# Optimization experiments

Measured on AMD Instinct MI355X. Metric: run time of the kernel, lower is better.

The kernel has to match this reference:

```python
import jax, jax.numpy as jnp
import numpy as np

D_MODEL, D_Q, D_K, D_V, N = 1024, 128, 128, 128, 8192

def setup_inputs() -> dict:
    key = jax.random.key(0)
    ks = jax.random.split(key, 7)
    s = 1.0 / np.sqrt(D_MODEL)
    return {
        "x": jax.random.normal(ks[0], (N, D_MODEL), dtype=jnp.float32),
        "Wq": jax.random.uniform(ks[1], (D_MODEL, D_Q), jnp.float32, -s, s),
        "bq": jax.random.uniform(ks[2], (D_Q,), jnp.float32, -s, s),
        "Wk": jax.random.uniform(ks[3], (D_MODEL, D_K), jnp.float32, -s, s),
        "bk": jax.random.uniform(ks[4], (D_K,), jnp.float32, -s, s),
        "Wv": jax.random.uniform(ks[5], (D_MODEL, D_V), jnp.float32, -s, s),
        "bv": jax.random.uniform(ks[6], (D_V,), jnp.float32, -s, s),
    }

def reference(x, Wq, bq, Wk, bk, Wv, bv):
    q = x @ Wq + bq          # [N, d_q]
    k = x @ Wk + bk          # [N, d_k]
    v = x @ Wv + bv          # [N, d_v]
    scale = jnp.sqrt(jnp.asarray(q.shape[-1], q.dtype))
    scores = (q @ k.T) / scale          # [N, N]
    attn = jax.nn.softmax(scores, axis=1)  # matches nn.Softmax(dim=1) on 2D
    return attn @ v                     # [N, d_v]
```

## Files before the change

kernel.cpp:

```cpp
#include <hip/hip_runtime.h>


typedef __attribute__((ext_vector_type(8))) short bf16x8;
typedef __attribute__((ext_vector_type(4))) float f32x4;

#define NTOK 8192
#define DMODEL 1024
#define DH 128
#define NSPLIT 8
#define CPS 16

__device__ __forceinline__ unsigned short f2bf(float f) {
  unsigned int u = __builtin_bit_cast(unsigned int, f);
  u += 0x7fffu + ((u >> 16) & 1u);
  return (unsigned short)(u >> 16);
}

__device__ __forceinline__ unsigned int pack2bf(float a, float b) {
  return (unsigned int)f2bf(a) | ((unsigned int)f2bf(b) << 16);
}

__device__ __forceinline__ void gl2lds16(const void* gp, void* lp) {
  const __attribute__((address_space(1))) unsigned int* g =
      (const __attribute__((address_space(1))) unsigned int*)gp;
  __attribute__((address_space(3))) unsigned int* l =
      (__attribute__((address_space(3))) unsigned int*)lp;
  __builtin_amdgcn_global_load_lds(g, l, 16, 0, 0);
}

__global__ __launch_bounds__(256) void k_prep(const float* __restrict__ x,
                                              const float* __restrict__ Wq,
                                              const float* __restrict__ Wk,
                                              const float* __restrict__ Wv,
                                              unsigned short* __restrict__ xb,
                                              unsigned short* __restrict__ wt) {
  __shared__ unsigned short tile[32 * 130];
  int bid = blockIdx.x;
  int t = threadIdx.x;
  if (bid < 4096) {
    int gid = bid * 256 + t;
    const float4* src = (const float4*)x;
    float4 a = src[2 * gid];
    float4 b = src[2 * gid + 1];
    union { unsigned short s[8]; uint4 v; } o;
    o.s[0] = f2bf(a.x); o.s[1] = f2bf(a.y); o.s[2] = f2bf(a.z); o.s[3] = f2bf(a.w);
    o.s[4] = f2bf(b.x); o.s[5] = f2bf(b.y); o.s[6] = f2bf(b.z); o.s[7] = f2bf(b.w);
    ((uint4*)xb)[gid] = o.v;
  } else {
    int b2 = bid - 4096;
    int p = b2 >> 5;
    int k0 = (b2 & 31) * 32;
    const float* W = (p == 0) ? Wq : ((p == 1) ? Wk : Wv);
    float vscale = (p == 2) ? 0.0625f : 1.0f;
#pragma unroll
    for (int i = 0; i < 16; i++) {
      int e = i * 256 + t;
      int n = e & 127, kk = e >> 7;
      tile[kk * 130 + n] = f2bf(W[(size_t)(k0 + kk) * DH + n] * vscale);
    }
    __syncthreads();
#pragma unroll
    for (int i = 0; i < 16; i++) {
      int e = i * 256 + t;
      int kk = e & 31, n = e >> 5;
      wt[(size_t)(p * DH + n) * DMODEL + k0 + kk] = tile[kk * 130 + n];
    }
  }
}

__global__ __launch_bounds__(256) void k_qkv(const unsigned short* __restrict__ xb,
                                             const unsigned short* __restrict__ wt,
                                             const float* __restrict__ bq,
                                             const float* __restrict__ bk,
                                             const float* __restrict__ bv,
                                             unsigned short* __restrict__ qs,
                                             unsigned short* __restrict__ kkv,
                                             unsigned short* __restrict__ vt) {
  __shared__ unsigned short xt[2][64 * 64];
  __shared__ unsigned short wtt[2][128 * 64];
  int p = blockIdx.x, mt = blockIdx.y;
  int tid = threadIdx.x;
  int w = tid >> 6, lane = tid & 63, l16 = lane & 15, g = lane >> 4;

#define STAGE_Q(buf, k0)                                                     \
  {                                                                          \
    _Pragma("unroll") for (int ii = 0; ii < 2; ii++) {                       \
      int i = w * 2 + ii;                                                    \
      int xrow = i * 8 + (lane >> 3);                                        \
      int xpc = (lane & 7) ^ (xrow & 7);                                     \
      gl2lds16(&xb[(size_t)(mt * 64 + xrow) * DMODEL + (k0) + xpc * 8],      \
               &xt[buf][i * 512]);                                           \
    }                                                                        \
    _Pragma("unroll") for (int ii = 0; ii < 4; ii++) {                       \
      int i = w * 4 + ii;                                                    \
      int wr = i * 8 + (lane >> 3);                                          \
      int wpc = (lane & 7) ^ (wr & 7);                                       \
      gl2lds16(&wt[(size_t)(p * DH + wr) * DMODEL + (k0) + wpc * 8],         \
               &wtt[buf][i * 512]);                                          \
    }                                                                        \
  }

  f32x4 zero = {0.f, 0.f, 0.f, 0.f};
  f32x4 acc[8];
#pragma unroll
  for (int i = 0; i < 8; i++) acc[i] = zero;

  STAGE_Q(0, 0);
  int arow = w * 16 + l16, r7 = l16 & 7;

  for (int kt2 = 0; kt2 < 16; kt2++) {
    int b = kt2 & 1;
    __syncthreads();
    if (kt2 < 15) STAGE_Q(b ^ 1, (kt2 + 1) * 64);

    bf16x8 a0 = *(const bf16x8*)&xt[b][arow * 64 + ((g ^ r7) & 7) * 8];
    bf16x8 a1 = *(const bf16x8*)&xt[b][arow * 64 + (((4 + g) ^ r7) & 7) * 8];
#pragma unroll
    for (int nt = 0; nt < 8; nt++) {
      int col = nt * 16 + l16;
      int c7 = col & 7;
      bf16x8 b0 = *(const bf16x8*)&wtt[b][col * 64 + ((g ^ c7) & 7) * 8];
      bf16x8 b1 = *(const bf16x8*)&wtt[b][col * 64 + (((4 + g) ^ c7) & 7) * 8];
      acc[nt] = __builtin_amdgcn_mfma_f32_16x16x32_bf16(a0, b0, acc[nt], 0, 0, 0);
      acc[nt] = __builtin_amdgcn_mfma_f32_16x16x32_bf16(a1, b1, acc[nt], 0, 0, 0);
    }
  }
#undef STAGE_Q

  const float* bias = (p == 0) ? bq : ((p == 1) ? bk : bv);
  float mult = (p == 0) ? (0.08838834764831845f * 1.44269504088896340f) : 1.0f;
  if (p < 2) {
    unsigned short* outp = (p == 0) ? qs : kkv;
#pragma unroll
    for (int nt = 0; nt < 8; nt++) {
      int col = nt * 16 + l16;
      float bsv = bias[col];
#pragma unroll
      for (int r = 0; r < 4; r++) {
        int row = mt * 64 + w * 16 + g * 4 + r;
        outp[(size_t)row * DH + col] = f2bf((acc[nt][r] + bsv) * mult);
      }
    }
  } else {
#pragma unroll
    for (int nt = 0; nt < 8; nt++) {
      int col = nt * 16 + l16;
      float bsv = bias[col] * 0.0625f;
      int row0 = mt * 64 + w * 16 + g * 4;
      uint2 uv;
      uv.x = pack2bf(acc[nt][0] + bsv, acc[nt][1] + bsv);
      uv.y = pack2bf(acc[nt][2] + bsv, acc[nt][3] + bsv);
      *(uint2*)(&vt[(size_t)col * NTOK + row0]) = uv;
    }
  }
}

__global__ __launch_bounds__(256, 2) void k_flash(const unsigned short* __restrict__ qs,
                                                  const unsigned short* __restrict__ kkv,
                                                  const unsigned short* __restrict__ vt,
                                                  _Float16* __restrict__ opart,
                                                  float* __restrict__ lpart) {
  __shared__ unsigned short kt[2][64 * 128];
  __shared__ unsigned short vtl[2][128 * 64];
  __shared__ unsigned short pscr[4 * 2 * 1024];
  int sp = blockIdx.x, qt = blockIdx.y;
  int tid = threadIdx.x;
  int w = tid >> 6, lane = tid & 63, l16 = lane & 15, g = lane >> 4;
  int swz2 = (l16 & 7) ^ ((l16 >> 3) << 1);

  bf16x8 qf[2][4];
  int qbase = qt * 128 + w * 32;
#pragma unroll
  for (int q2 = 0; q2 < 2; q2++)
#pragma unroll
    for (int f = 0; f < 4; f++)
      qf[q2][f] = *(const bf16x8*)(&qs[(size_t)(qbase + q2 * 16 + l16) * DH + f * 32 + g * 8]);

  int pcK[4], pcV[2], pcP[2];
#pragma unroll
  for (int f = 0; f < 4; f++) {
    int lc = f * 4 + g;
    pcK[f] = (lc & 8) | ((lc ^ l16) & 7);
  }
#pragma unroll
  for (int kb = 0; kb < 2; kb++) {
    int lc = kb * 4 + g;
    pcV[kb] = (lc ^ l16) & 7;
    pcP[kb] = (lc ^ swz2) & 7;
  }

#define STAGE_FLASH(buf, chunk)                                                 \
  {                                                                             \
    int key0 = (chunk) * 64;                                                    \
    _Pragma("unroll") for (int ii = 0; ii < 4; ii++) {                          \
      int i = w * 4 + ii;                                                       \
      int krow = 4 * i + (lane >> 4);                                           \
      int klc = ((lane & 15) & 8) | (((lane & 15) ^ krow) & 7);                 \
      gl2lds16(&kkv[(size_t)(key0 + krow) * DH + klc * 8], &kt[buf][i * 512]);  \
      int vrow = 8 * i + (lane >> 3);                                           \
      int vlc = ((lane & 7) ^ vrow) & 7;                                        \
      gl2lds16(&vt[(size_t)vrow * NTOK + key0 + vlc * 8], &vtl[buf][i * 512]);  \
    }                                                                           \
  }

  f32x4 zero = {0.f, 0.f, 0.f, 0.f};
  f32x4 o[2][8];
#pragma unroll
  for (int q2 = 0; q2 < 2; q2++)
#pragma unroll
    for (int dt = 0; dt < 8; dt++) o[q2][dt] = zero;
  float l[2] = {0.f, 0.f};

  int c0 = sp * CPS;
  STAGE_FLASH(0, c0);

  for (int it = 0; it < CPS; it++) {
    int b = it & 1;
    __syncthreads();
    if (it + 1 < CPS) STAGE_FLASH(b ^ 1, c0 + it + 1);

    f32x4 s[2][4];
#pragma unroll
    for (int q2 = 0; q2 < 2; q2++)
#pragma unroll
      for (int mt = 0; mt < 4; mt++) s[q2][mt] = zero;
#pragma unroll
    for (int mt = 0; mt < 4; mt++) {
      bf16x8 kf[4];
#pragma unroll
      for (int f = 0; f < 4; f++)
        kf[f] = *(const bf16x8*)(&kt[b][(mt * 16 + l16) * 128 + pcK[f] * 8]);
#pragma unroll
      for (int f = 0; f < 4; f++) {
        s[0][mt] = __builtin_amdgcn_mfma_f32_16x16x32_bf16(kf[f], qf[0][f], s[0][mt], 0, 0, 0);
        s[1][mt] = __builtin_amdgcn_mfma_f32_16x16x32_bf16(kf[f], qf[1][f], s[1][mt], 0, 0, 0);
      }
    }

#pragma unroll
    for (int q2 = 0; q2 < 2; q2++) {
      unsigned short* pw = &pscr[(w * 2 + q2) * 1024];
      float ssum = 0.f;
#pragma unroll
      for (int mt = 0; mt < 4; mt++) {
        float p0 = __builtin_amdgcn_exp2f(s[q2][mt][0]);
        float p1 = __builtin_amdgcn_exp2f(s[q2][mt][1]);
        float p2 = __builtin_amdgcn_exp2f(s[q2][mt][2]);
        float p3 = __builtin_amdgcn_exp2f(s[q2][mt][3]);
        ssum += (p0 + p1) + (p2 + p3);
        uint2 uv;
        uv.x = pack2bf(p0, p1);
        uv.y = pack2bf(p2, p3);
        int ch = ((mt * 2 + (g >> 1)) ^ swz2) & 7;
        *(uint2*)(&pw[l16 * 64 + ch * 8 + (g & 1) * 4]) = uv;
      }
      l[q2] += ssum;
    }

    bf16x8 pb[2][2];
#pragma unroll
    for (int q2 = 0; q2 < 2; q2++)
#pragma unroll
      for (int kb = 0; kb < 2; kb++)
        pb[q2][kb] = *(const bf16x8*)(&pscr[(w * 2 + q2) * 1024 + l16 * 64 + pcP[kb] * 8]);

#pragma unroll
    for (int dt = 0; dt < 8; dt++)
#pragma unroll
      for (int kb = 0; kb < 2; kb++) {
        bf16x8 vf = *(const bf16x8*)(&vtl[b][(dt * 16 + l16) * 64 + pcV[kb] * 8]);
        o[0][dt] = __builtin_amdgcn_mfma_f32_16x16x32_bf16(vf, pb[0][kb], o[0][dt], 0, 0, 0);
        o[1][dt] = __builtin_amdgcn_mfma_f32_16x16x32_bf16(vf, pb[1][kb], o[1][dt], 0, 0, 0);
      }
  }
#undef STAGE_FLASH

#pragma unroll
  for (int q2 = 0; q2 < 2; q2++) {
    l[q2] += __shfl_xor(l[q2], 16);
    l[q2] += __shfl_xor(l[q2], 32);
    int qrow = qbase + q2 * 16 + l16;
    size_t obase = ((size_t)sp * NTOK + qrow) * DH;
#pragma unroll
    for (int dt = 0; dt < 8; dt++) {
      union { _Float16 h[4]; uint2 u; } pk;
      pk.h[0] = (_Float16)o[q2][dt][0];
      pk.h[1] = (_Float16)o[q2][dt][1];
      pk.h[2] = (_Float16)o[q2][dt][2];
      pk.h[3] = (_Float16)o[q2][dt][3];
      *(uint2*)(&opart[obase + dt * 16 + g * 4]) = pk.u;
    }
    if (g == 0) lpart[sp * NTOK + qrow] = l[q2];
  }
}

__global__ __launch_bounds__(256) void k_merge(const _Float16* __restrict__ opart,
                                               const float* __restrict__ lpart,
                                               float* __restrict__ out) {
  int gid = blockIdx.x * 256 + threadIdx.x;
  int row = gid >> 6, cp = gid & 63;
  float den = 0.f, n0 = 0.f, n1 = 0.f;
#pragma unroll
  for (int s = 0; s < NSPLIT; s++) {
    den += lpart[s * NTOK + row];
    union { unsigned int u; _Float16 h[2]; } v;
    v.u = *(const unsigned int*)&opart[((size_t)s * NTOK + row) * DH + cp * 2];
    n0 += (float)v.h[0];
    n1 += (float)v.h[1];
  }
  float inv = 16.0f / den;
  *(float2*)&out[(size_t)row * DH + cp * 2] = make_float2(n0 * inv, n1 * inv);
}

extern "C" void kernel_launch(void* const* d_in, const int* in_sizes, int n_in,
                              void* d_out, int out_size, void* d_ws, size_t ws_size,
                              hipStream_t stream) {
  const float* x  = (const float*)d_in[0];
  const float* Wq = (const float*)d_in[1];
  const float* bq = (const float*)d_in[2];
  const float* Wk = (const float*)d_in[3];
  const float* bk = (const float*)d_in[4];
  const float* Wv = (const float*)d_in[5];
  const float* bv = (const float*)d_in[6];
  float* out = (float*)d_out;

  char* ws = (char*)d_ws;
  unsigned short* xb    = (unsigned short*)(ws);
  _Float16*       opart = (_Float16*)(ws);
  unsigned short* wt  = (unsigned short*)(ws + 16777216);
  unsigned short* qsb = (unsigned short*)(ws + 17563648);
  unsigned short* kkb = (unsigned short*)(ws + 19660800);
  unsigned short* vtb = (unsigned short*)(ws + 21757952);
  float* lpart = (float*)(ws + 23855104);

  k_prep<<<4192, 256, 0, stream>>>(x, Wq, Wk, Wv, xb, wt);
  k_qkv<<<dim3(3, 128), 256, 0, stream>>>(xb, wt, bq, bk, bv, qsb, kkb, vtb);
  k_flash<<<dim3(NSPLIT, 64), 256, 0, stream>>>(qsb, kkb, vtb, opart, lpart);
  k_merge<<<2048, 256, 0, stream>>>(opart, lpart, out);
}
```

Baseline: 158.2 us.

## Shrink flash key chunks to 32 and raise split count and occupancy

Halves the per-iteration key/value tile in the flash kernel from 64 to 32 keys and reworks the LDS swizzles and the padded P scratch to match. This cuts shared memory per block, so launch bounds rise from 2 to 3 blocks per CU. The key range is now split 12 ways instead of 8, with uneven chunk boundaries, to fill the extra slots. Workspace offsets move to fit the larger partial-output buffer. In exchange there are more barriers per key processed, more partial outputs for the merge kernel to combine, and tighter register limits.

```diff
diff --git a/kernel.cpp b/kernel.cpp
--- a/kernel.cpp
+++ b/kernel.cpp
@@ -7,8 +7,8 @@
 #define NTOK 8192
 #define DMODEL 1024
 #define DH 128
-#define NSPLIT 8
-#define CPS 16
+#define NSPLIT 12
+#define NCH32 256
 
 __device__ __forceinline__ unsigned short f2bf(float f) {
   unsigned int u = __builtin_bit_cast(unsigned int, f);
@@ -155,18 +155,18 @@
   }
 }
 
-__global__ __launch_bounds__(256, 2) void k_flash(const unsigned short* __restrict__ qs,
+__global__ __launch_bounds__(256, 3) void k_flash(const unsigned short* __restrict__ qs,
                                                   const unsigned short* __restrict__ kkv,
                                                   const unsigned short* __restrict__ vt,
                                                   _Float16* __restrict__ opart,
                                                   float* __restrict__ lpart) {
-  __shared__ unsigned short kt[2][64 * 128];
-  __shared__ unsigned short vtl[2][128 * 64];
-  __shared__ unsigned short pscr[4 * 2 * 1024];
+  __shared__ unsigned short kt[2][32 * 128];
+  __shared__ unsigned short vtl[2][128 * 32];
+  __shared__ unsigned short pscr[4 * 2 * 640];
   int sp = blockIdx.x, qt = blockIdx.y;
   int tid = threadIdx.x;
   int w = tid >> 6, lane = tid & 63, l16 = lane & 15, g = lane >> 4;
-  int swz2 = (l16 & 7) ^ ((l16 >> 3) << 1);
+  int l3 = l16 & 3;
 
   bf16x8 qf[2][4];
   int qbase = qt * 128 + w * 32;
@@ -176,31 +176,27 @@
     for (int f = 0; f < 4; f++)
       qf[q2][f] = *(const bf16x8*)(&qs[(size_t)(qbase + q2 * 16 + l16) * DH + f * 32 + g * 8]);
 
-  int pcK[4], pcV[2], pcP[2];
+  int pcK[4];
 #pragma unroll
   for (int f = 0; f < 4; f++) {
     int lc = f * 4 + g;
     pcK[f] = (lc & 8) | ((lc ^ l16) & 7);
   }
-#pragma unroll
-  for (int kb = 0; kb < 2; kb++) {
-    int lc = kb * 4 + g;
-    pcV[kb] = (lc ^ l16) & 7;
-    pcP[kb] = (lc ^ swz2) & 7;
-  }
-
-#define STAGE_FLASH(buf, chunk)                                                 \
-  {                                                                             \
-    int key0 = (chunk) * 64;                                                    \
-    _Pragma("unroll") for (int ii = 0; ii < 4; ii++) {                          \
-      int i = w * 4 + ii;                                                       \
-      int krow = 4 * i + (lane >> 4);                                           \
-      int klc = ((lane & 15) & 8) | (((lane & 15) ^ krow) & 7);                 \
-      gl2lds16(&kkv[(size_t)(key0 + krow) * DH + klc * 8], &kt[buf][i * 512]);  \
-      int vrow = 8 * i + (lane >> 3);                                           \
-      int vlc = ((lane & 7) ^ vrow) & 7;                                        \
-      gl2lds16(&vt[(size_t)vrow * NTOK + key0 + vlc * 8], &vtl[buf][i * 512]);  \
-    }                                                                           \
+  int pcV = (g ^ l3) & 3;
+  int pcP = (g ^ l3) & 3;
+
+#define STAGE_FL(buf, chunk)                                                     \
+  {                                                                              \
+    int key0s = (chunk) * 32;                                                    \
+    _Pragma("unroll") for (int ii = 0; ii < 2; ii++) {                           \
+      int i = w * 2 + ii;                                                        \
+      int krow = 4 * i + (lane >> 4);                                            \
+      int klc = ((lane & 15) & 8) | (((lane & 15) ^ krow) & 7);                  \
+      gl2lds16(&kkv[(size_t)(key0s + krow) * DH + klc * 8], &kt[buf][i * 512]);  \
+      int vrow = 16 * i + (lane >> 2);                                           \
+      int vlc = ((lane & 3) ^ (vrow & 3)) & 3;                                   \
+      gl2lds16(&vt[(size_t)vrow * NTOK + key0s + vlc * 8], &vtl[buf][i * 512]);  \
+    }                                                                            \
   }
 
   f32x4 zero = {0.f, 0.f, 0.f, 0.f};
@@ -210,22 +206,25 @@
 #pragma unroll
     for (int dt = 0; dt < 8; dt++) o[q2][dt] = zero;
   float l[2] = {0.f, 0.f};
-
-  int c0 = sp * CPS;
-  STAGE_FLASH(0, c0);
-
-  for (int it = 0; it < CPS; it++) {
-    int b = it & 1;
+  unsigned short* pw0 = &pscr[(w * 2 + 0) * 640];
+  unsigned short* pw1 = &pscr[(w * 2 + 1) * 640];
+
+  int c0 = (sp * NCH32) / NSPLIT;
+  int c1 = ((sp + 1) * NCH32) / NSPLIT;
+  STAGE_FL(0, c0);
+
+  for (int it = c0; it < c1; it++) {
+    int b = (it - c0) & 1;
     __syncthreads();
-    if (it + 1 < CPS) STAGE_FLASH(b ^ 1, c0 + it + 1);
-
-    f32x4 s[2][4];
+    if (it + 1 < c1) STAGE_FL(b ^ 1, it + 1);
+
+    f32x4 s[2][2];
 #pragma unroll
     for (int q2 = 0; q2 < 2; q2++)
 #pragma unroll
-      for (int mt = 0; mt < 4; mt++) s[q2][mt] = zero;
-#pragma unroll
-    for (int mt = 0; mt < 4; mt++) {
+      for (int mt = 0; mt < 2; mt++) s[q2][mt] = zero;
+#pragma unroll
+    for (int mt = 0; mt < 2; mt++) {
       bf16x8 kf[4];
 #pragma unroll
       for (int f = 0; f < 4; f++)
@@ -239,10 +238,10 @@
 
 #pragma unroll
     for (int q2 = 0; q2 < 2; q2++) {
-      unsigned short* pw = &pscr[(w * 2 + q2) * 1024];
+      unsigned short* pw = q2 ? pw1 : pw0;
       float ssum = 0.f;
 #pragma unroll
-      for (int mt = 0; mt < 4; mt++) {
+      for (int mt = 0; mt < 2; mt++) {
         float p0 = __builtin_amdgcn_exp2f(s[q2][mt][0]);
         float p1 = __builtin_amdgcn_exp2f(s[q2][mt][1]);
         float p2 = __builtin_amdgcn_exp2f(s[q2][mt][2]);
@@ -251,29 +250,23 @@
         uint2 uv;
         uv.x = pack2bf(p0, p1);
         uv.y = pack2bf(p2, p3);
-        int ch = ((mt * 2 + (g >> 1)) ^ swz2) & 7;
-        *(uint2*)(&pw[l16 * 64 + ch * 8 + (g & 1) * 4]) = uv;
+        int ck = ((mt * 2 + (g >> 1)) ^ l3) & 3;
+        *(uint2*)(&pw[l16 * 40 + ck * 8 + (g & 1) * 4]) = uv;
       }
       l[q2] += ssum;
     }
 
-    bf16x8 pb[2][2];
-#pragma unroll
-    for (int q2 = 0; q2 < 2; q2++)
-#pragma unroll
-      for (int kb = 0; kb < 2; kb++)
-        pb[q2][kb] = *(const bf16x8*)(&pscr[(w * 2 + q2) * 1024 + l16 * 64 + pcP[kb] * 8]);
-
-#pragma unroll
-    for (int dt = 0; dt < 8; dt++)
-#pragma unroll
-      for (int kb = 0; kb < 2; kb++) {
-        bf16x8 vf = *(const bf16x8*)(&vtl[b][(dt * 16 + l16) * 64 + pcV[kb] * 8]);
-        o[0][dt] = __builtin_amdgcn_mfma_f32_16x16x32_bf16(vf, pb[0][kb], o[0][dt], 0, 0, 0);
-        o[1][dt] = __builtin_amdgcn_mfma_f32_16x16x32_bf16(vf, pb[1][kb], o[1][dt], 0, 0, 0);
-      }
-  }
-#undef STAGE_FLASH
+    bf16x8 pb0 = *(const bf16x8*)(&pw0[l16 * 40 + pcP * 8]);
+    bf16x8 pb1 = *(const bf16x8*)(&pw1[l16 * 40 + pcP * 8]);
+
+#pragma unroll
+    for (int dt = 0; dt < 8; dt++) {
+      bf16x8 vf = *(const bf16x8*)(&vtl[b][(dt * 16 + l16) * 32 + pcV * 8]);
+      o[0][dt] = __builtin_amdgcn_mfma_f32_16x16x32_bf16(vf, pb0, o[0][dt], 0, 0, 0);
+      o[1][dt] = __builtin_amdgcn_mfma_f32_16x16x32_bf16(vf, pb1, o[1][dt], 0, 0, 0);
+    }
+  }
+#undef STAGE_FL
 
 #pragma unroll
   for (int q2 = 0; q2 < 2; q2++) {
@@ -327,11 +320,11 @@
   char* ws = (char*)d_ws;
   unsigned short* xb    = (unsigned short*)(ws);
   _Float16*       opart = (_Float16*)(ws);
-  unsigned short* wt  = (unsigned short*)(ws + 16777216);
-  unsigned short* qsb = (unsigned short*)(ws + 17563648);
-  unsigned short* kkb = (unsigned short*)(ws + 19660800);
-  unsigned short* vtb = (unsigned short*)(ws + 21757952);
-  float* lpart = (float*)(ws + 23855104);
+  unsigned short* wt  = (unsigned short*)(ws + 25165824);
+  unsigned short* qsb = (unsigned short*)(ws + 25952256);
+  unsigned short* kkb = (unsigned short*)(ws + 28049408);
+  unsigned short* vtb = (unsigned short*)(ws + 30146560);
+  float* lpart = (float*)(ws + 32243712);
 
   k_prep<<<4192, 256, 0, stream>>>(x, Wq, Wk, Wv, xb, wt);
   k_qkv<<<dim3(3, 128), 256, 0, stream>>>(xb, wt, bq, bk, bv, qsb, kkb, vtb);
```

Measured after the change: 167.2 us. +5.7%, slower.
